# Optimization experiments

Measured on AMD Instinct MI355X. Metric: run time of the kernel, lower is better.

Reference implementation:

```python
import jax, jax.numpy as jnp
import numpy as np

KEY_DIM = 64  # scaling uses key_dim, NOT the full projection dim (faithful to source)


def setup_inputs() -> dict:
    key = jax.random.key(0)
    ks = jax.random.split(key, 9)
    B, S, D = 4, 4096, 512
    P = 512  # heads * key_dim = 8 * 64
    s = 0.02
    return {
        "x": jax.random.normal(ks[0], (B, S, D), jnp.float32),
        "Wq": jax.random.normal(ks[1], (D, P), jnp.float32) * s,
        "bq": jnp.zeros((P,), jnp.float32),
        "Wk": jax.random.normal(ks[2], (D, P), jnp.float32) * s,
        "bk": jnp.zeros((P,), jnp.float32),
        "Wv": jax.random.normal(ks[3], (D, P), jnp.float32) * s,
        "bv": jnp.zeros((P,), jnp.float32),
        "Wo": jax.random.normal(ks[4], (P, D), jnp.float32) * s,
        "bo": jnp.zeros((D,), jnp.float32),
    }


def reference(x, Wq, bq, Wk, bk, Wv, bv, Wo, bo):
    # Manual QKV projections over the FULL heads*key_dim dim (no head split,
    # exactly as the original layer).
    q = jnp.einsum("bsd,dp->bsp", x, Wq) + bq
    k = jnp.einsum("bsd,dp->bsp", x, Wk) + bk
    v = jnp.einsum("bsd,dp->bsp", x, Wv) + bv
    scale = 1.0 / jnp.sqrt(jnp.float32(KEY_DIM))
    scores = jnp.einsum("bsp,btp->bst", q, k) * scale  # [B,S,S]
    attn = jax.nn.softmax(scores, axis=-1)
    attended = jnp.einsum("bst,btp->bsp", attn, v)
    return jnp.einsum("bsp,pd->bsd", attended, Wo) + bo
```

## Files before the change

### kernel.cpp

```cpp
#include <hip/hip_runtime.h>
#include <hip/hip_bf16.h>

typedef __bf16 bf16x8 __attribute__((ext_vector_type(8)));
typedef float  floatx4 __attribute__((ext_vector_type(4)));

#define MFMA16(a, b, c) __builtin_amdgcn_mfma_f32_16x16x32_bf16((a), (b), (c), 0, 0, 0)

static constexpr int BATCH = 4;
static constexpr int SEQ   = 4096;
static constexpr int MTOT  = BATCH * SEQ;

__device__ __forceinline__ void gload16(const void* gsrc, void* ldst)
{
    auto* g = reinterpret_cast<const __attribute__((address_space(1))) unsigned int*>(
        reinterpret_cast<unsigned long long>(gsrc));
    auto* l = reinterpret_cast<__attribute__((address_space(3))) unsigned int*>(
        reinterpret_cast<unsigned long long>(ldst));
    __builtin_amdgcn_global_load_lds(g, l, 16, 0, 0);
}

__global__ __launch_bounds__(256) void cvt_x(
    const float* __restrict__ x, __bf16* __restrict__ xb)
{
    const size_t i = ((size_t)blockIdx.x * 256 + threadIdx.x) * 8;
    const float4 a = *reinterpret_cast<const float4*>(x + i);
    const float4 c = *reinterpret_cast<const float4*>(x + i + 4);
    bf16x8 r;
    r[0] = (__bf16)a.x; r[1] = (__bf16)a.y; r[2] = (__bf16)a.z; r[3] = (__bf16)a.w;
    r[4] = (__bf16)c.x; r[5] = (__bf16)c.y; r[6] = (__bf16)c.z; r[7] = (__bf16)c.w;
    *reinterpret_cast<bf16x8*>(xb + i) = r;
}

__global__ __launch_bounds__(256) void transpose_w(
    const float* __restrict__ W, __bf16* __restrict__ WT)
{
    __shared__ __bf16 tile[64 * 68];
    const int t   = blockIdx.x;
    const int k0  = (t >> 3) * 64;
    const int n0  = (t & 7) * 64;
    const int tid = threadIdx.x;
#pragma unroll
    for (int it = 0; it < 4; ++it) {
        const int flat = it * 1024 + tid * 4;
        const int r = flat >> 6;
        const int c = flat & 63;
        const float4 v = *reinterpret_cast<const float4*>(
            W + (size_t)(k0 + r) * 512 + n0 + c);
        tile[r * 68 + c + 0] = (__bf16)v.x;
        tile[r * 68 + c + 1] = (__bf16)v.y;
        tile[r * 68 + c + 2] = (__bf16)v.z;
        tile[r * 68 + c + 3] = (__bf16)v.w;
    }
    __syncthreads();
#pragma unroll
    for (int it = 0; it < 2; ++it) {
        const int gid = it * 256 + tid;
        const int n  = gid >> 3;
        const int k8 = (gid & 7) * 8;
        bf16x8 r8;
#pragma unroll
        for (int j = 0; j < 8; ++j) r8[j] = tile[(k8 + j) * 68 + n];
        *reinterpret_cast<bf16x8*>(WT + (size_t)(n0 + n) * 512 + k0 + k8) = r8;
    }
}

__global__ __launch_bounds__(256, 2) void qkv_gemm(
    const __bf16* __restrict__ xb,
    const __bf16* __restrict__ WqT, const float* __restrict__ bq,
    const __bf16* __restrict__ WkT, const float* __restrict__ bk,
    const __bf16* __restrict__ WvT, const float* __restrict__ bv,
    __bf16* __restrict__ qb, __bf16* __restrict__ kb, __bf16* __restrict__ vbT)
{
    __shared__ __attribute__((aligned(16))) __bf16 As[64 * 64];
    __shared__ __attribute__((aligned(16))) __bf16 Bq[64 * 64];
    __shared__ __attribute__((aligned(16))) __bf16 Bk[64 * 64];
    __shared__ __attribute__((aligned(16))) __bf16 Bv[64 * 64];
    __shared__ __bf16 Cs[64 * 80];

    const int tid  = threadIdx.x;
    const int w    = tid >> 6;
    const int lane = tid & 63;
    const int quad = lane >> 4;
    const int l15  = lane & 15;
    const int fid  = blockIdx.x;
    const int n0   = (fid & 7) * 64;
    const int m0   = (fid >> 3) * 64;

    const int srow0 = w * 8 + (lane >> 3);
    const int sgrp  = lane & 7;

    floatx4 aq[4], ak[4], av[4];
#pragma unroll
    for (int nt = 0; nt < 4; ++nt) {
        aq[nt] = floatx4{0.f, 0.f, 0.f, 0.f};
        ak[nt] = floatx4{0.f, 0.f, 0.f, 0.f};
        av[nt] = floatx4{0.f, 0.f, 0.f, 0.f};
    }

    for (int k0 = 0; k0 < 512; k0 += 64) {
#pragma unroll
        for (int i = 0; i < 2; ++i) {
            const int r  = i * 32 + srow0;
            const int cg = (sgrp ^ (r & 7)) << 3;
            const int db = (i * 32 + w * 8) * 64;
            gload16(xb  + (size_t)(m0 + r) * 512 + k0 + cg, &As[db]);
            gload16(WqT + (size_t)(n0 + r) * 512 + k0 + cg, &Bq[db]);
            gload16(WkT + (size_t)(n0 + r) * 512 + k0 + cg, &Bk[db]);
            gload16(WvT + (size_t)(n0 + r) * 512 + k0 + cg, &Bv[db]);
        }
        __syncthreads();

#pragma unroll
        for (int kk = 0; kk < 2; ++kk) {
            const int arow = w * 16 + l15;
            const bf16x8 af = *reinterpret_cast<const bf16x8*>(
                &As[arow * 64 + (((kk * 4 + quad) ^ (arow & 7)) << 3)]);
#pragma unroll
            for (int nt = 0; nt < 4; ++nt) {
                const int brow = nt * 16 + l15;
                const int off  = brow * 64 + (((kk * 4 + quad) ^ (brow & 7)) << 3);
                aq[nt] = MFMA16(af, *reinterpret_cast<const bf16x8*>(&Bq[off]), aq[nt]);
                ak[nt] = MFMA16(af, *reinterpret_cast<const bf16x8*>(&Bk[off]), ak[nt]);
                av[nt] = MFMA16(af, *reinterpret_cast<const bf16x8*>(&Bv[off]), av[nt]);
            }
        }
        __syncthreads();
    }

#pragma unroll
    for (int nt = 0; nt < 4; ++nt) {
        const int col = n0 + nt * 16 + l15;
        const float bqv = bq[col], bkv = bk[col], bvv = bv[col];
#pragma unroll
        for (int r = 0; r < 4; ++r) {
            const int row = m0 + w * 16 + quad * 4 + r;
            qb[(size_t)row * 512 + col] = (__bf16)((aq[nt][r] + bqv) * 0.125f);
            kb[(size_t)row * 512 + col] = (__bf16)(ak[nt][r] + bkv);
            Cs[(nt * 16 + l15) * 80 + w * 16 + quad * 4 + r] = (__bf16)(av[nt][r] + bvv);
        }
    }
    __syncthreads();
    {
        const int bb = m0 >> 12;
        const int tb = m0 & 4095;
        __bf16* yb = vbT + (size_t)bb * 512 * 4096;
#pragma unroll
        for (int it = 0; it < 2; ++it) {
            const int flat = it * 2048 + tid * 8;
            const int pl = flat >> 6;
            const int c  = flat & 63;
            const bf16x8 vv = *reinterpret_cast<const bf16x8*>(&Cs[pl * 80 + c]);
            *reinterpret_cast<bf16x8*>(&yb[(size_t)(n0 + pl) * 4096 + tb + c]) = vv;
        }
    }
}

__global__ __launch_bounds__(256, 2) void out_gemm(
    const __bf16* __restrict__ A, const __bf16* __restrict__ WT,
    const float* __restrict__ bias, float* __restrict__ Y)
{
    __shared__ __attribute__((aligned(16))) __bf16 As[64 * 64];
    __shared__ __attribute__((aligned(16))) __bf16 Bs[64 * 64];

    const int tid  = threadIdx.x;
    const int w    = tid >> 6;
    const int lane = tid & 63;
    const int quad = lane >> 4;
    const int l15  = lane & 15;
    const int fid  = blockIdx.x;
    const int n0   = (fid & 7) * 64;
    const int m0   = (fid >> 3) * 64;

    const int srow0 = w * 8 + (lane >> 3);
    const int sgrp  = lane & 7;

    floatx4 acc[4];
#pragma unroll
    for (int nt = 0; nt < 4; ++nt) acc[nt] = floatx4{0.f, 0.f, 0.f, 0.f};

    for (int k0 = 0; k0 < 512; k0 += 64) {
#pragma unroll
        for (int i = 0; i < 2; ++i) {
            const int r  = i * 32 + srow0;
            const int cg = (sgrp ^ (r & 7)) << 3;
            const int db = (i * 32 + w * 8) * 64;
            gload16(A  + (size_t)(m0 + r) * 512 + k0 + cg, &As[db]);
            gload16(WT + (size_t)(n0 + r) * 512 + k0 + cg, &Bs[db]);
        }
        __syncthreads();

#pragma unroll
        for (int kk = 0; kk < 2; ++kk) {
            const int arow = w * 16 + l15;
            const bf16x8 af = *reinterpret_cast<const bf16x8*>(
                &As[arow * 64 + (((kk * 4 + quad) ^ (arow & 7)) << 3)]);
#pragma unroll
            for (int nt = 0; nt < 4; ++nt) {
                const int brow = nt * 16 + l15;
                const bf16x8 bfv = *reinterpret_cast<const bf16x8*>(
                    &Bs[brow * 64 + (((kk * 4 + quad) ^ (brow & 7)) << 3)]);
                acc[nt] = MFMA16(af, bfv, acc[nt]);
            }
        }
        __syncthreads();
    }

#pragma unroll
    for (int nt = 0; nt < 4; ++nt) {
        const int col = n0 + nt * 16 + l15;
        const float bv = bias[col];
#pragma unroll
        for (int r = 0; r < 4; ++r) {
            const int row = m0 + w * 16 + quad * 4 + r;
            Y[(size_t)row * 512 + col] = acc[nt][r] + bv;
        }
    }
}

__global__ __launch_bounds__(256, 2) void flash_attn(
    const __bf16* __restrict__ q, const __bf16* __restrict__ k,
    const __bf16* __restrict__ vT, __bf16* __restrict__ pO,
    float* __restrict__ lP)
{
    __shared__ __attribute__((aligned(16))) __bf16 Kt[32 * 520];
    __shared__ __attribute__((aligned(16))) __bf16 Vt[512 * 32];
    __shared__ __attribute__((aligned(16))) __bf16 Pl[4 * 16 * 40];

    const int tid  = threadIdx.x;
    const int w    = tid >> 6;
    const int lane = tid & 63;
    const int quad = lane >> 4;
    const int l15  = lane & 15;

    const int fid = blockIdx.x;
    const int g   = fid & 7;
    const int hb  = g & 1;
    const int b   = g >> 1;
    const int q0  = (fid >> 3) * 64;
    const size_t boff = (size_t)b * SEQ * 512;

    bf16x8 qf[16];
    {
        const __bf16* qrow = q + boff + (size_t)(q0 + w * 16 + l15) * 512;
#pragma unroll
        for (int kk = 0; kk < 16; ++kk)
            qf[kk] = *reinterpret_cast<const bf16x8*>(qrow + kk * 32 + quad * 8);
    }

    floatx4 o[32];
#pragma unroll
    for (int i = 0; i < 32; ++i) o[i] = floatx4{0.f, 0.f, 0.f, 0.f};
    float lsum[4] = {0.f, 0.f, 0.f, 0.f};

    const __bf16* kB  = k + boff;
    const __bf16* vTb = vT + boff;
    const int tstart = hb * 2048;
    const int tend   = tstart + 2048;

    const int vprow = lane >> 2;
    const int vkoff = (((lane & 3) ^ ((lane >> 3) & 3)) << 3);

    {
        const __bf16* kbase = kB + (size_t)(tstart + w * 8) * 512 + lane * 8;
#pragma unroll
        for (int j = 0; j < 8; ++j)
            gload16(kbase + (size_t)j * 512, &Kt[(w * 8 + j) * 520]);
#pragma unroll
        for (int j = 0; j < 8; ++j) {
            const int p0 = (w * 8 + j) * 16;
            gload16(vTb + (size_t)(p0 + vprow) * 4096 + tstart + vkoff, &Vt[p0 * 32]);
        }
    }

    for (int t0 = tstart; t0 < tend; t0 += 32) {
        const int tn = (t0 + 32 < tend) ? t0 + 32 : t0;

        asm volatile("s_waitcnt vmcnt(8)" ::: "memory");
        __builtin_amdgcn_s_barrier();

        floatx4 sa0 = floatx4{0.f, 0.f, 0.f, 0.f};
        floatx4 sa1 = floatx4{0.f, 0.f, 0.f, 0.f};
        __builtin_amdgcn_s_setprio(1);
#pragma unroll
        for (int kk = 0; kk < 16; ++kk) {
            const bf16x8 kf0 = *reinterpret_cast<const bf16x8*>(
                &Kt[l15 * 520 + kk * 32 + quad * 8]);
            const bf16x8 kf1 = *reinterpret_cast<const bf16x8*>(
                &Kt[(16 + l15) * 520 + kk * 32 + quad * 8]);
            sa0 = MFMA16(qf[kk], kf0, sa0);
            sa1 = MFMA16(qf[kk], kf1, sa1);
        }
        __builtin_amdgcn_s_setprio(0);

#pragma unroll
        for (int r = 0; r < 4; ++r) {
            const float p0 = __expf(sa0[r]);
            const float p1 = __expf(sa1[r]);
            lsum[r] += p0 + p1;
            Pl[(w * 16 + quad * 4 + r) * 40 + l15]      = (__bf16)p0;
            Pl[(w * 16 + quad * 4 + r) * 40 + 16 + l15] = (__bf16)p1;
        }

        __builtin_amdgcn_s_barrier();

        {
            const __bf16* kbase = kB + (size_t)(tn + w * 8) * 512 + lane * 8;
#pragma unroll
            for (int j = 0; j < 8; ++j)
                gload16(kbase + (size_t)j * 512, &Kt[(w * 8 + j) * 520]);
        }

        asm volatile("s_waitcnt vmcnt(8)" ::: "memory");
        __builtin_amdgcn_s_barrier();

        const bf16x8 pf = *reinterpret_cast<const bf16x8*>(
            &Pl[(w * 16 + l15) * 40 + quad * 8]);
        const int vsw = ((quad ^ ((l15 >> 1) & 3)) << 3);
        __builtin_amdgcn_s_setprio(1);
#pragma unroll
        for (int pt = 0; pt < 32; ++pt) {
            const bf16x8 vf = *reinterpret_cast<const bf16x8*>(
                &Vt[(pt * 16 + l15) * 32 + vsw]);
            o[pt] = MFMA16(pf, vf, o[pt]);
        }
        __builtin_amdgcn_s_setprio(0);

        __builtin_amdgcn_s_barrier();

#pragma unroll
        for (int j = 0; j < 8; ++j) {
            const int p0 = (w * 8 + j) * 16;
            gload16(vTb + (size_t)(p0 + vprow) * 4096 + tn + vkoff, &Vt[p0 * 32]);
        }
    }
    asm volatile("s_waitcnt vmcnt(0)" ::: "memory");

#pragma unroll
    for (int r = 0; r < 4; ++r) {
#pragma unroll
        for (int off = 1; off < 16; off <<= 1)
            lsum[r] += __shfl_xor(lsum[r], off);
    }
    const int rowbase = b * SEQ + q0 + w * 16 + quad * 4;
    if (l15 == 0) {
#pragma unroll
        for (int r = 0; r < 4; ++r)
            lP[(size_t)hb * MTOT + rowbase + r] = lsum[r];
    }
    __bf16* pOh = pO + (size_t)hb * MTOT * 512;
#pragma unroll
    for (int pt = 0; pt < 32; ++pt) {
#pragma unroll
        for (int r = 0; r < 4; ++r)
            pOh[(size_t)(rowbase + r) * 512 + pt * 16 + l15] = (__bf16)o[pt][r];
    }
}

__global__ __launch_bounds__(256) void merge_attn(
    const __bf16* __restrict__ pO, const float* __restrict__ lP,
    __bf16* __restrict__ att)
{
    const int gidx = blockIdx.x * 256 + threadIdx.x;
    const int row  = gidx >> 6;
    const int c8   = (gidx & 63) * 8;
    const float li = 1.0f / (lP[row] + lP[MTOT + row]);
    const bf16x8 a = *reinterpret_cast<const bf16x8*>(&pO[(size_t)row * 512 + c8]);
    const bf16x8 bvv = *reinterpret_cast<const bf16x8*>(
        &pO[((size_t)MTOT + row) * 512 + c8]);
    bf16x8 r8;
#pragma unroll
    for (int j = 0; j < 8; ++j)
        r8[j] = (__bf16)(((float)a[j] + (float)bvv[j]) * li);
    *reinterpret_cast<bf16x8*>(&att[(size_t)row * 512 + c8]) = r8;
}

extern "C" void kernel_launch(void* const* d_in, const int* in_sizes, int n_in,
                              void* d_out, int out_size, void* d_ws, size_t ws_size,
                              hipStream_t stream)
{
    (void)in_sizes; (void)n_in; (void)out_size; (void)ws_size;

    const float* x  = (const float*)d_in[0];
    const float* Wq = (const float*)d_in[1];
    const float* bq = (const float*)d_in[2];
    const float* Wk = (const float*)d_in[3];
    const float* bk = (const float*)d_in[4];
    const float* Wv = (const float*)d_in[5];
    const float* bv = (const float*)d_in[6];
    const float* Wo = (const float*)d_in[7];
    const float* bo = (const float*)d_in[8];
    float* out = (float*)d_out;

    __bf16* qb  = (__bf16*)d_ws;
    __bf16* kb  = qb  + (size_t)MTOT * 512;
    __bf16* vbT = kb  + (size_t)MTOT * 512;
    float*  lP  = (float*)(vbT + (size_t)MTOT * 512);
    __bf16* pO  = (__bf16*)d_out;
    __bf16* ab  = qb;

    __bf16* xb  = (__bf16*)d_out;
    __bf16* WqT = xb  + (size_t)MTOT * 512;
    __bf16* WkT = WqT + 512 * 512;
    __bf16* WvT = WkT + 512 * 512;
    __bf16* WoT = kb;

    cvt_x<<<MTOT * 512 / 2048, 256, 0, stream>>>(x, xb);
    transpose_w<<<64, 256, 0, stream>>>(Wq, WqT);
    transpose_w<<<64, 256, 0, stream>>>(Wk, WkT);
    transpose_w<<<64, 256, 0, stream>>>(Wv, WvT);

    qkv_gemm<<<2048, 256, 0, stream>>>(xb, WqT, bq, WkT, bk, WvT, bv, qb, kb, vbT);

    flash_attn<<<512, 256, 0, stream>>>(qb, kb, vbT, pO, lP);

    transpose_w<<<64, 256, 0, stream>>>(Wo, WoT);
    merge_attn<<<MTOT * 64 / 256, 256, 0, stream>>>(pO, lP, ab);

    out_gemm<<<2048, 256, 0, stream>>>(ab, WoT, bo, out);
}
```

Measured before the change: 359.5 us.

## Switch flash attention to 32x32 MFMA with fragment-packed Q/K/V layouts

The QKV projection now writes Q, K and V directly in a pre-swizzled fragment-major layout so the attention kernel can load whole MFMA operand fragments with contiguous 16-byte loads. The attention kernel moves from 16x16x32 to 32x32x16 bf16 MFMA, with 64-key tiles split across wave pairs, a larger LDS staging buffer and an LDS-staged coalesced output write. The aim is fewer LDS reads per MFMA FLOP and less swizzle arithmetic. In exchange, occupancy drops to one block per CU, since launch bounds go from 2 to 1 and LDS use grows to about 136KB.

New measurement: 379.1 us. 5.5% more time.

```diff
diff --git a/kernel.cpp b/kernel.cpp
--- a/kernel.cpp
+++ b/kernel.cpp
@@ -3,8 +3,10 @@
 
 typedef __bf16 bf16x8 __attribute__((ext_vector_type(8)));
 typedef float  floatx4 __attribute__((ext_vector_type(4)));
+typedef float  floatx16 __attribute__((ext_vector_type(16)));
 
 #define MFMA16(a, b, c) __builtin_amdgcn_mfma_f32_16x16x32_bf16((a), (b), (c), 0, 0, 0)
+#define MFMA32(a, b, c) __builtin_amdgcn_mfma_f32_32x32x16_bf16((a), (b), (c), 0, 0, 0)
 
 static constexpr int BATCH = 4;
 static constexpr int SEQ   = 4096;
@@ -69,7 +71,7 @@
     const __bf16* __restrict__ WqT, const float* __restrict__ bq,
     const __bf16* __restrict__ WkT, const float* __restrict__ bk,
     const __bf16* __restrict__ WvT, const float* __restrict__ bv,
-    __bf16* __restrict__ qb, __bf16* __restrict__ kb, __bf16* __restrict__ vbT)
+    __bf16* __restrict__ qb, __bf16* __restrict__ kb, __bf16* __restrict__ vb)
 {
     __shared__ __attribute__((aligned(16))) __bf16 As[64 * 64];
     __shared__ __attribute__((aligned(16))) __bf16 Bq[64 * 64];
@@ -127,30 +129,40 @@
         __syncthreads();
     }
 
+    const int b64q = (m0 >> 12) * 64 + ((m0 & 4095) >> 6);
 #pragma unroll
     for (int nt = 0; nt < 4; ++nt) {
-        const int col = n0 + nt * 16 + l15;
+        const int col   = n0 + nt * 16 + l15;
+        const int s_col = col >> 4;
+        const int hcol  = l15 >> 3;
+        const int jcol  = l15 & 7;
         const float bqv = bq[col], bkv = bk[col], bvv = bv[col];
 #pragma unroll
         for (int r = 0; r < 4; ++r) {
-            const int row = m0 + w * 16 + quad * 4 + r;
-            qb[(size_t)row * 512 + col] = (__bf16)((aq[nt][r] + bqv) * 0.125f);
-            kb[(size_t)row * 512 + col] = (__bf16)(ak[nt][r] + bkv);
-            Cs[(nt * 16 + l15) * 80 + w * 16 + quad * 4 + r] = (__bf16)(av[nt][r] + bvv);
+            const int rr   = w * 16 + quad * 4 + r;
+            const int lrow = rr & 31;
+            const int rbt  = rr >> 5;
+            const size_t qe = ((size_t)((b64q * 2 + rbt) * 32 + s_col) << 9)
+                            + ((hcol * 32 + lrow) << 3) + jcol;
+            const size_t ke = ((size_t)(b64q * 64 + rbt * 32 + s_col) << 9)
+                            + ((hcol * 32 + lrow) << 3) + jcol;
+            qb[qe] = (__bf16)((aq[nt][r] + bqv) * 0.125f);
+            kb[ke] = (__bf16)(ak[nt][r] + bkv);
+            Cs[(nt * 16 + l15) * 80 + rr] = (__bf16)(av[nt][r] + bvv);
         }
     }
     __syncthreads();
     {
-        const int bb = m0 >> 12;
-        const int tb = m0 & 4095;
-        __bf16* yb = vbT + (size_t)bb * 512 * 4096;
 #pragma unroll
         for (int it = 0; it < 2; ++it) {
             const int flat = it * 2048 + tid * 8;
             const int pl = flat >> 6;
             const int c  = flat & 63;
             const bf16x8 vv = *reinterpret_cast<const bf16x8*>(&Cs[pl * 80 + c]);
-            *reinterpret_cast<bf16x8*>(&yb[(size_t)(n0 + pl) * 4096 + tb + c]) = vv;
+            const int p = n0 + pl;
+            const size_t ve = ((size_t)(b64q * 64 + (p >> 5) * 4 + (c >> 4)) << 9)
+                            + ((((c >> 3) & 1) * 32 + (p & 31)) << 3);
+            *reinterpret_cast<bf16x8*>(vb + ve) = vv;
         }
     }
 }
@@ -217,142 +229,160 @@
     }
 }
 
-__global__ __launch_bounds__(256, 2) void flash_attn(
-    const __bf16* __restrict__ q, const __bf16* __restrict__ k,
-    const __bf16* __restrict__ vT, __bf16* __restrict__ pO,
+__global__ __launch_bounds__(256, 1) void flash_attn(
+    const __bf16* __restrict__ qfg, const __bf16* __restrict__ kfg,
+    const __bf16* __restrict__ vfg, __bf16* __restrict__ pO,
     float* __restrict__ lP)
 {
-    __shared__ __attribute__((aligned(16))) __bf16 Kt[32 * 520];
-    __shared__ __attribute__((aligned(16))) __bf16 Vt[512 * 32];
-    __shared__ __attribute__((aligned(16))) __bf16 Pl[4 * 16 * 40];
+    __shared__ __attribute__((aligned(16))) __bf16 SH[69632];
+    __bf16* Kf = SH;
+    __bf16* Vf = SH + 32768;
+    __bf16* Pf = SH + 65536;
 
     const int tid  = threadIdx.x;
     const int w    = tid >> 6;
     const int lane = tid & 63;
-    const int quad = lane >> 4;
-    const int l15  = lane & 15;
-
-    const int fid = blockIdx.x;
-    const int g   = fid & 7;
-    const int hb  = g & 1;
-    const int b   = g >> 1;
-    const int q0  = (fid >> 3) * 64;
-    const size_t boff = (size_t)b * SEQ * 512;
-
-    bf16x8 qf[16];
+    const int l31  = lane & 31;
+    const int h    = lane >> 5;
+
+    const int fid  = blockIdx.x;
+    const int g    = fid & 7;
+    const int hb   = g & 1;
+    const int b    = g >> 1;
+    const int qblk = fid >> 3;
+    const int kb   = w & 1;
+    const int rb   = w >> 1;
+
+    bf16x8 qf[32];
     {
-        const __bf16* qrow = q + boff + (size_t)(q0 + w * 16 + l15) * 512;
-#pragma unroll
-        for (int kk = 0; kk < 16; ++kk)
-            qf[kk] = *reinterpret_cast<const bf16x8*>(qrow + kk * 32 + quad * 8);
-    }
-
-    floatx4 o[32];
-#pragma unroll
-    for (int i = 0; i < 32; ++i) o[i] = floatx4{0.f, 0.f, 0.f, 0.f};
-    float lsum[4] = {0.f, 0.f, 0.f, 0.f};
-
-    const __bf16* kB  = k + boff;
-    const __bf16* vTb = vT + boff;
-    const int tstart = hb * 2048;
-    const int tend   = tstart + 2048;
-
-    const int vprow = lane >> 2;
-    const int vkoff = (((lane & 3) ^ ((lane >> 3) & 3)) << 3);
-
-    {
-        const __bf16* kbase = kB + (size_t)(tstart + w * 8) * 512 + lane * 8;
-#pragma unroll
-        for (int j = 0; j < 8; ++j)
-            gload16(kbase + (size_t)j * 512, &Kt[(w * 8 + j) * 520]);
-#pragma unroll
-        for (int j = 0; j < 8; ++j) {
-            const int p0 = (w * 8 + j) * 16;
-            gload16(vTb + (size_t)(p0 + vprow) * 4096 + tstart + vkoff, &Vt[p0 * 32]);
-        }
-    }
-
-    for (int t0 = tstart; t0 < tend; t0 += 32) {
-        const int tn = (t0 + 32 < tend) ? t0 + 32 : t0;
-
-        asm volatile("s_waitcnt vmcnt(8)" ::: "memory");
+        const __bf16* qbase = qfg + ((size_t)((b * 64 + qblk) * 2 + rb) << 14)
+                                  + (lane << 3);
+#pragma unroll
+        for (int s = 0; s < 32; ++s)
+            qf[s] = *reinterpret_cast<const bf16x8*>(qbase + (s << 9));
+    }
+
+    floatx16 o[4][2];
+#pragma unroll
+    for (int pb = 0; pb < 4; ++pb)
+#pragma unroll
+        for (int r2 = 0; r2 < 2; ++r2)
+#pragma unroll
+            for (int r = 0; r < 16; ++r) o[pb][r2][r] = 0.f;
+    float lsum = 0.f;
+
+    auto issueK = [&](int tt) {
+        const __bf16* src = kfg + ((size_t)(b * 64 + tt) << 15)
+                                + ((w * 16) << 9) + (lane << 3);
+#pragma unroll
+        for (int j = 0; j < 16; ++j)
+            gload16(src + (j << 9), &Kf[(w * 16 + j) << 9]);
+    };
+    auto issueV = [&](int tt) {
+        const __bf16* src = vfg + ((size_t)(b * 64 + tt) << 15)
+                                + ((w * 16) << 9) + (lane << 3);
+#pragma unroll
+        for (int j = 0; j < 16; ++j)
+            gload16(src + (j << 9), &Vf[(w * 16 + j) << 9]);
+    };
+
+    const int tt0 = hb * 32;
+    issueK(tt0);
+    issueV(tt0);
+
+#pragma unroll 1
+    for (int i = 0; i < 32; ++i) {
+        const int tt = tt0 + i;
+        (void)tt;
+
+        asm volatile("s_waitcnt vmcnt(16)" ::: "memory");
         __builtin_amdgcn_s_barrier();
 
-        floatx4 sa0 = floatx4{0.f, 0.f, 0.f, 0.f};
-        floatx4 sa1 = floatx4{0.f, 0.f, 0.f, 0.f};
+        floatx16 s0, s1;
+#pragma unroll
+        for (int r = 0; r < 16; ++r) { s0[r] = 0.f; s1[r] = 0.f; }
         __builtin_amdgcn_s_setprio(1);
 #pragma unroll
-        for (int kk = 0; kk < 16; ++kk) {
-            const bf16x8 kf0 = *reinterpret_cast<const bf16x8*>(
-                &Kt[l15 * 520 + kk * 32 + quad * 8]);
-            const bf16x8 kf1 = *reinterpret_cast<const bf16x8*>(
-                &Kt[(16 + l15) * 520 + kk * 32 + quad * 8]);
-            sa0 = MFMA16(qf[kk], kf0, sa0);
-            sa1 = MFMA16(qf[kk], kf1, sa1);
+        for (int s = 0; s < 32; s += 2) {
+            const bf16x8 a0 = *reinterpret_cast<const bf16x8*>(
+                &Kf[((kb * 32 + s) << 9) + (lane << 3)]);
+            s0 = MFMA32(a0, qf[s], s0);
+            const bf16x8 a1 = *reinterpret_cast<const bf16x8*>(
+                &Kf[((kb * 32 + s + 1) << 9) + (lane << 3)]);
+            s1 = MFMA32(a1, qf[s + 1], s1);
         }
         __builtin_amdgcn_s_setprio(0);
-
-#pragma unroll
-        for (int r = 0; r < 4; ++r) {
-            const float p0 = __expf(sa0[r]);
-            const float p1 = __expf(sa1[r]);
-            lsum[r] += p0 + p1;
-            Pl[(w * 16 + quad * 4 + r) * 40 + l15]      = (__bf16)p0;
-            Pl[(w * 16 + quad * 4 + r) * 40 + 16 + l15] = (__bf16)p1;
-        }
-
+        const floatx16 sv = s0 + s1;
+
+#pragma unroll
+        for (int r = 0; r < 16; ++r) {
+            const float pv = __expf(sv[r]);
+            lsum += pv;
+            Pf[((rb * 4 + kb * 2 + (r >> 3)) << 9) + (((r >> 2) & 1) << 8)
+               + (l31 << 3) + (r & 3) + 4 * h] = (__bf16)pv;
+        }
+        asm volatile("s_waitcnt lgkmcnt(0)" ::: "memory");
         __builtin_amdgcn_s_barrier();
 
-        {
-            const __bf16* kbase = kB + (size_t)(tn + w * 8) * 512 + lane * 8;
-#pragma unroll
-            for (int j = 0; j < 8; ++j)
-                gload16(kbase + (size_t)j * 512, &Kt[(w * 8 + j) * 520]);
-        }
-
-        asm volatile("s_waitcnt vmcnt(8)" ::: "memory");
-        __builtin_amdgcn_s_barrier();
-
-        const bf16x8 pf = *reinterpret_cast<const bf16x8*>(
-            &Pl[(w * 16 + l15) * 40 + quad * 8]);
-        const int vsw = ((quad ^ ((l15 >> 1) & 3)) << 3);
+        if (i + 1 < 32) {
+            issueK(tt0 + i + 1);
+            asm volatile("s_waitcnt vmcnt(16)" ::: "memory");
+        } else {
+            asm volatile("s_waitcnt vmcnt(0)" ::: "memory");
+        }
+
         __builtin_amdgcn_s_setprio(1);
 #pragma unroll
-        for (int pt = 0; pt < 32; ++pt) {
-            const bf16x8 vf = *reinterpret_cast<const bf16x8*>(
-                &Vt[(pt * 16 + l15) * 32 + vsw]);
-            o[pt] = MFMA16(pf, vf, o[pt]);
+        for (int ks = 0; ks < 4; ++ks) {
+            const bf16x8 p0 = *reinterpret_cast<const bf16x8*>(
+                &Pf[(ks << 9) + (lane << 3)]);
+            const bf16x8 p1 = *reinterpret_cast<const bf16x8*>(
+                &Pf[((4 + ks) << 9) + (lane << 3)]);
+#pragma unroll
+            for (int pb = 0; pb < 4; ++pb) {
+                const bf16x8 av = *reinterpret_cast<const bf16x8*>(
+                    &Vf[((w * 16 + pb * 4 + ks) << 9) + (lane << 3)]);
+                o[pb][0] = MFMA32(av, p0, o[pb][0]);
+                o[pb][1] = MFMA32(av, p1, o[pb][1]);
+            }
         }
         __builtin_amdgcn_s_setprio(0);
 
-        __builtin_amdgcn_s_barrier();
-
-#pragma unroll
-        for (int j = 0; j < 8; ++j) {
-            const int p0 = (w * 8 + j) * 16;
-            gload16(vTb + (size_t)(p0 + vprow) * 4096 + tn + vkoff, &Vt[p0 * 32]);
-        }
-    }
-    asm volatile("s_waitcnt vmcnt(0)" ::: "memory");
-
-#pragma unroll
-    for (int r = 0; r < 4; ++r) {
-#pragma unroll
-        for (int off = 1; off < 16; off <<= 1)
-            lsum[r] += __shfl_xor(lsum[r], off);
-    }
-    const int rowbase = b * SEQ + q0 + w * 16 + quad * 4;
-    if (l15 == 0) {
-#pragma unroll
-        for (int r = 0; r < 4; ++r)
-            lP[(size_t)hb * MTOT + rowbase + r] = lsum[r];
-    }
-    __bf16* pOh = pO + (size_t)hb * MTOT * 512;
-#pragma unroll
-    for (int pt = 0; pt < 32; ++pt) {
-#pragma unroll
-        for (int r = 0; r < 4; ++r)
-            pOh[(size_t)(rowbase + r) * 512 + pt * 16 + l15] = (__bf16)o[pt][r];
+        if (i + 1 < 32) issueV(tt0 + i + 1);
+    }
+
+    __builtin_amdgcn_s_barrier();
+
+    lsum += __shfl_xor(lsum, 32);
+    float* Ls = (float*)Pf;
+    if (lane < 32) Ls[w * 32 + l31] = lsum;
+
+    __bf16* Ot = SH;
+#pragma unroll
+    for (int pb = 0; pb < 4; ++pb)
+#pragma unroll
+        for (int r2 = 0; r2 < 2; ++r2)
+#pragma unroll
+            for (int r = 0; r < 16; ++r)
+                Ot[(r2 * 32 + l31) * 520 + w * 128 + pb * 32
+                   + (r & 3) + ((r >> 2) << 3) + 4 * h] = (__bf16)o[pb][r2][r];
+
+    asm volatile("s_waitcnt lgkmcnt(0)" ::: "memory");
+    __builtin_amdgcn_s_barrier();
+
+    const int rowbase = b * SEQ + qblk * 64;
+    if (w < 2 && lane < 32)
+        lP[(size_t)hb * MTOT + rowbase + w * 32 + l31] =
+            Ls[(w * 2) * 32 + l31] + Ls[(w * 2 + 1) * 32 + l31];
+
+    __bf16* pOh = pO + ((size_t)hb * MTOT << 9);
+#pragma unroll
+    for (int it = 0; it < 16; ++it) {
+        const int id  = it * 256 + tid;
+        const int row = id >> 6;
+        const int gg  = id & 63;
+        *reinterpret_cast<bf16x8*>(pOh + (size_t)(rowbase + row) * 512 + gg * 8) =
+            *reinterpret_cast<const bf16x8*>(&Ot[row * 520 + gg * 8]);
     }
 }
 
@@ -393,8 +423,8 @@
 
     __bf16* qb  = (__bf16*)d_ws;
     __bf16* kb  = qb  + (size_t)MTOT * 512;
-    __bf16* vbT = kb  + (size_t)MTOT * 512;
-    float*  lP  = (float*)(vbT + (size_t)MTOT * 512);
+    __bf16* vb  = kb  + (size_t)MTOT * 512;
+    float*  lP  = (float*)(vb + (size_t)MTOT * 512);
     __bf16* pO  = (__bf16*)d_out;
     __bf16* ab  = qb;
 
@@ -409,9 +439,9 @@
     transpose_w<<<64, 256, 0, stream>>>(Wk, WkT);
     transpose_w<<<64, 256, 0, stream>>>(Wv, WvT);
 
-    qkv_gemm<<<2048, 256, 0, stream>>>(xb, WqT, bq, WkT, bk, WvT, bv, qb, kb, vbT);
-
-    flash_attn<<<512, 256, 0, stream>>>(qb, kb, vbT, pO, lP);
+    qkv_gemm<<<2048, 256, 0, stream>>>(xb, WqT, bq, WkT, bk, WvT, bv, qb, kb, vb);
+
+    flash_attn<<<512, 256, 0, stream>>>(qb, kb, vb, pO, lP);
 
     transpose_w<<<64, 256, 0, stream>>>(Wo, WoT);
     merge_attn<<<MTOT * 64 / 256, 256, 0, stream>>>(pO, lP, ab);
```

## Split PV matmul by output columns per wave and stage output via LDS

Applied to the files above, without the earlier changes.

The P·V stage now gives each wave its own 128-column slice of V for all 64 query rows, instead of every wave reading all 512 V columns for its own 16 rows. Each wave loads 8 V fragments into registers once and reuses them across 4 P row-blocks, with the MFMA operands swapped. This cuts LDS traffic for V at the cost of reading P from every wave's rows. The output is transposed through shared memory so the global store becomes coalesced 16-byte row writes, which adds extra barriers and an LDS round trip at the end.

Result: slower. 466.3 us (+29.7%).

```diff
diff --git a/kernel.cpp b/kernel.cpp
--- a/kernel.cpp
+++ b/kernel.cpp
@@ -222,9 +222,10 @@
     const __bf16* __restrict__ vT, __bf16* __restrict__ pO,
     float* __restrict__ lP)
 {
-    __shared__ __attribute__((aligned(16))) __bf16 Kt[32 * 520];
-    __shared__ __attribute__((aligned(16))) __bf16 Vt[512 * 32];
-    __shared__ __attribute__((aligned(16))) __bf16 Pl[4 * 16 * 40];
+    __shared__ __attribute__((aligned(16))) __bf16 SH[35584];
+    __bf16* Kt = SH;
+    __bf16* Vt = SH + 16640;
+    __bf16* Pl = SH + 33024;
 
     const int tid  = threadIdx.x;
     const int w    = tid >> 6;
@@ -259,6 +260,7 @@
 
     const int vprow = lane >> 2;
     const int vkoff = (((lane & 3) ^ ((lane >> 3) & 3)) << 3);
+    const int vsw   = ((quad ^ ((l15 >> 1) & 3)) << 3);
 
     {
         const __bf16* kbase = kB + (size_t)(tstart + w * 8) * 512 + lane * 8;
@@ -301,6 +303,7 @@
             Pl[(w * 16 + quad * 4 + r) * 40 + 16 + l15] = (__bf16)p1;
         }
 
+        asm volatile("s_waitcnt lgkmcnt(0)" ::: "memory");
         __builtin_amdgcn_s_barrier();
 
         {
@@ -313,15 +316,20 @@
         asm volatile("s_waitcnt vmcnt(8)" ::: "memory");
         __builtin_amdgcn_s_barrier();
 
-        const bf16x8 pf = *reinterpret_cast<const bf16x8*>(
-            &Pl[(w * 16 + l15) * 40 + quad * 8]);
-        const int vsw = ((quad ^ ((l15 >> 1) & 3)) << 3);
+        bf16x8 vfr[8];
+#pragma unroll
+        for (int pb = 0; pb < 8; ++pb)
+            vfr[pb] = *reinterpret_cast<const bf16x8*>(
+                &Vt[((w * 8 + pb) * 16 + l15) * 32 + vsw]);
+
         __builtin_amdgcn_s_setprio(1);
 #pragma unroll
-        for (int pt = 0; pt < 32; ++pt) {
-            const bf16x8 vf = *reinterpret_cast<const bf16x8*>(
-                &Vt[(pt * 16 + l15) * 32 + vsw]);
-            o[pt] = MFMA16(pf, vf, o[pt]);
+        for (int rb = 0; rb < 4; ++rb) {
+            const bf16x8 pf = *reinterpret_cast<const bf16x8*>(
+                &Pl[(rb * 16 + l15) * 40 + quad * 8]);
+#pragma unroll
+            for (int pb = 0; pb < 8; ++pb)
+                o[pb * 4 + rb] = MFMA16(vfr[pb], pf, o[pb * 4 + rb]);
         }
         __builtin_amdgcn_s_setprio(0);
 
@@ -341,18 +349,38 @@
         for (int off = 1; off < 16; off <<= 1)
             lsum[r] += __shfl_xor(lsum[r], off);
     }
-    const int rowbase = b * SEQ + q0 + w * 16 + quad * 4;
+    const int lrowbase = b * SEQ + q0 + w * 16 + quad * 4;
     if (l15 == 0) {
 #pragma unroll
         for (int r = 0; r < 4; ++r)
-            lP[(size_t)hb * MTOT + rowbase + r] = lsum[r];
-    }
+            lP[(size_t)hb * MTOT + lrowbase + r] = lsum[r];
+    }
+
+    __builtin_amdgcn_s_barrier();
+    __bf16* Ot = SH;
+#pragma unroll
+    for (int rb = 0; rb < 4; ++rb) {
+#pragma unroll
+        for (int pb = 0; pb < 8; ++pb) {
+#pragma unroll
+            for (int r = 0; r < 4; ++r)
+                Ot[(rb * 16 + l15) * 520 + (w * 8 + pb) * 16 + quad * 4 + r] =
+                    (__bf16)o[pb * 4 + rb][r];
+        }
+    }
+    asm volatile("s_waitcnt lgkmcnt(0)" ::: "memory");
+    __builtin_amdgcn_s_barrier();
+
     __bf16* pOh = pO + (size_t)hb * MTOT * 512;
-#pragma unroll
-    for (int pt = 0; pt < 32; ++pt) {
-#pragma unroll
-        for (int r = 0; r < 4; ++r)
-            pOh[(size_t)(rowbase + r) * 512 + pt * 16 + l15] = (__bf16)o[pt][r];
+    const int prowbase = b * SEQ + q0;
+#pragma unroll
+    for (int it = 0; it < 16; ++it) {
+        const int id  = it * 256 + tid;
+        const int row = id >> 6;
+        const int c8  = (id & 63) * 8;
+        *reinterpret_cast<bf16x8*>(
+            pOh + (size_t)(prowbase + row) * 512 + c8) =
+            *reinterpret_cast<const bf16x8*>(&Ot[row * 520 + c8]);
     }
 }
 
```

## Enlarge flash-attention tiles to 128 queries and 64 keys per block

Applied to the files above, without the earlier changes.

The attention kernel now runs 512-thread blocks covering 128 query rows, so each K/V tile loaded into LDS is shared by eight waves instead of four. The key step per iteration doubles to 64, giving each wave four score MFMAs and two PV MFMAs per output tile, with a wider 8-way V swizzle and bigger P staging. The aim is to halve global K/V traffic and cut the number of barriers per key processed. In exchange it uses about 150 KB of LDS at one block per CU, and the grid drops to 256 blocks, which may leave the GPU underoccupied.

New measurement: 720.4 us. 100% more time.

```diff
diff --git a/kernel.cpp b/kernel.cpp
--- a/kernel.cpp
+++ b/kernel.cpp
@@ -217,14 +217,15 @@
     }
 }
 
-__global__ __launch_bounds__(256, 2) void flash_attn(
+__global__ __launch_bounds__(512, 1) void flash_attn(
     const __bf16* __restrict__ q, const __bf16* __restrict__ k,
     const __bf16* __restrict__ vT, __bf16* __restrict__ pO,
     float* __restrict__ lP)
 {
-    __shared__ __attribute__((aligned(16))) __bf16 Kt[32 * 520];
-    __shared__ __attribute__((aligned(16))) __bf16 Vt[512 * 32];
-    __shared__ __attribute__((aligned(16))) __bf16 Pl[4 * 16 * 40];
+    __shared__ __attribute__((aligned(16))) __bf16 SH[75264];
+    __bf16* Kt = SH;
+    __bf16* Vt = SH + 33280;
+    __bf16* Pl = SH + 66048;
 
     const int tid  = threadIdx.x;
     const int w    = tid >> 6;
@@ -236,7 +237,7 @@
     const int g   = fid & 7;
     const int hb  = g & 1;
     const int b   = g >> 1;
-    const int q0  = (fid >> 3) * 64;
+    const int q0  = (fid >> 3) * 128;
     const size_t boff = (size_t)b * SEQ * 512;
 
     bf16x8 qf[16];
@@ -257,81 +258,84 @@
     const int tstart = hb * 2048;
     const int tend   = tstart + 2048;
 
-    const int vprow = lane >> 2;
-    const int vkoff = (((lane & 3) ^ ((lane >> 3) & 3)) << 3);
-
-    {
-        const __bf16* kbase = kB + (size_t)(tstart + w * 8) * 512 + lane * 8;
+    const int vrow8 = lane >> 3;
+    const int vkoff = (((lane & 7) ^ vrow8) << 3);
+
+    auto issueK = [&](int t0) {
+        const __bf16* kbase = kB + (size_t)(t0 + w * 8) * 512 + lane * 8;
 #pragma unroll
         for (int j = 0; j < 8; ++j)
             gload16(kbase + (size_t)j * 512, &Kt[(w * 8 + j) * 520]);
+    };
+    auto issueV = [&](int t0) {
 #pragma unroll
         for (int j = 0; j < 8; ++j) {
-            const int p0 = (w * 8 + j) * 16;
-            gload16(vTb + (size_t)(p0 + vprow) * 4096 + tstart + vkoff, &Vt[p0 * 32]);
-        }
-    }
-
-    for (int t0 = tstart; t0 < tend; t0 += 32) {
-        const int tn = (t0 + 32 < tend) ? t0 + 32 : t0;
+            const int p0 = (w * 8 + j) * 8;
+            gload16(vTb + (size_t)(p0 + vrow8) * 4096 + t0 + vkoff, &Vt[p0 * 64]);
+        }
+    };
+
+    issueK(tstart);
+    issueV(tstart);
+
+    for (int t0 = tstart; t0 < tend; t0 += 64) {
+        const int tn = (t0 + 64 < tend) ? t0 + 64 : t0;
 
         asm volatile("s_waitcnt vmcnt(8)" ::: "memory");
         __builtin_amdgcn_s_barrier();
 
-        floatx4 sa0 = floatx4{0.f, 0.f, 0.f, 0.f};
-        floatx4 sa1 = floatx4{0.f, 0.f, 0.f, 0.f};
+        floatx4 sa[4];
+#pragma unroll
+        for (int nt = 0; nt < 4; ++nt) sa[nt] = floatx4{0.f, 0.f, 0.f, 0.f};
         __builtin_amdgcn_s_setprio(1);
 #pragma unroll
         for (int kk = 0; kk < 16; ++kk) {
-            const bf16x8 kf0 = *reinterpret_cast<const bf16x8*>(
-                &Kt[l15 * 520 + kk * 32 + quad * 8]);
-            const bf16x8 kf1 = *reinterpret_cast<const bf16x8*>(
-                &Kt[(16 + l15) * 520 + kk * 32 + quad * 8]);
-            sa0 = MFMA16(qf[kk], kf0, sa0);
-            sa1 = MFMA16(qf[kk], kf1, sa1);
+#pragma unroll
+            for (int nt = 0; nt < 4; ++nt) {
+                const bf16x8 kf = *reinterpret_cast<const bf16x8*>(
+                    &Kt[(nt * 16 + l15) * 520 + kk * 32 + quad * 8]);
+                sa[nt] = MFMA16(qf[kk], kf, sa[nt]);
+            }
         }
         __builtin_amdgcn_s_setprio(0);
 
 #pragma unroll
-        for (int r = 0; r < 4; ++r) {
-            const float p0 = __expf(sa0[r]);
-            const float p1 = __expf(sa1[r]);
-            lsum[r] += p0 + p1;
-            Pl[(w * 16 + quad * 4 + r) * 40 + l15]      = (__bf16)p0;
-            Pl[(w * 16 + quad * 4 + r) * 40 + 16 + l15] = (__bf16)p1;
+        for (int nt = 0; nt < 4; ++nt) {
+#pragma unroll
+            for (int r = 0; r < 4; ++r) {
+                const float pv = __expf(sa[nt][r]);
+                lsum[r] += pv;
+                Pl[(w * 16 + quad * 4 + r) * 72 + nt * 16 + l15] = (__bf16)pv;
+            }
         }
 
         __builtin_amdgcn_s_barrier();
 
-        {
-            const __bf16* kbase = kB + (size_t)(tn + w * 8) * 512 + lane * 8;
-#pragma unroll
-            for (int j = 0; j < 8; ++j)
-                gload16(kbase + (size_t)j * 512, &Kt[(w * 8 + j) * 520]);
-        }
+        issueK(tn);
 
         asm volatile("s_waitcnt vmcnt(8)" ::: "memory");
         __builtin_amdgcn_s_barrier();
 
-        const bf16x8 pf = *reinterpret_cast<const bf16x8*>(
-            &Pl[(w * 16 + l15) * 40 + quad * 8]);
-        const int vsw = ((quad ^ ((l15 >> 1) & 3)) << 3);
+        const bf16x8 pf0 = *reinterpret_cast<const bf16x8*>(
+            &Pl[(w * 16 + l15) * 72 + quad * 8]);
+        const bf16x8 pf1 = *reinterpret_cast<const bf16x8*>(
+            &Pl[(w * 16 + l15) * 72 + 32 + quad * 8]);
+        const int sw0 = ((quad ^ (l15 & 7)) << 3);
+        const int sw1 = (((4 + quad) ^ (l15 & 7)) << 3);
         __builtin_amdgcn_s_setprio(1);
 #pragma unroll
         for (int pt = 0; pt < 32; ++pt) {
-            const bf16x8 vf = *reinterpret_cast<const bf16x8*>(
-                &Vt[(pt * 16 + l15) * 32 + vsw]);
-            o[pt] = MFMA16(pf, vf, o[pt]);
+            const int row = (pt * 16 + l15) * 64;
+            const bf16x8 vf0 = *reinterpret_cast<const bf16x8*>(&Vt[row + sw0]);
+            const bf16x8 vf1 = *reinterpret_cast<const bf16x8*>(&Vt[row + sw1]);
+            o[pt] = MFMA16(pf0, vf0, o[pt]);
+            o[pt] = MFMA16(pf1, vf1, o[pt]);
         }
         __builtin_amdgcn_s_setprio(0);
 
         __builtin_amdgcn_s_barrier();
 
-#pragma unroll
-        for (int j = 0; j < 8; ++j) {
-            const int p0 = (w * 8 + j) * 16;
-            gload16(vTb + (size_t)(p0 + vprow) * 4096 + tn + vkoff, &Vt[p0 * 32]);
-        }
+        issueV(tn);
     }
     asm volatile("s_waitcnt vmcnt(0)" ::: "memory");
 
@@ -411,7 +415,7 @@
 
     qkv_gemm<<<2048, 256, 0, stream>>>(xb, WqT, bq, WkT, bk, WvT, bv, qb, kb, vbT);
 
-    flash_attn<<<512, 256, 0, stream>>>(qb, kb, vbT, pO, lP);
+    flash_attn<<<256, 512, 0, stream>>>(qb, kb, vbT, pO, lP);
 
     transpose_w<<<64, 256, 0, stream>>>(Wo, WoT);
     merge_attn<<<MTOT * 64 / 256, 256, 0, stream>>>(pO, lP, ab);
```
